# Kernel optimization log

Measured on AMD Instinct MI355X. Metric: run time of the kernel, lower is better.

Reference implementation:

```python
import jax, jax.numpy as jnp
import numpy as np

N = 9            # digits
NC = N * N       # 81 cells
H = 128          # hidden1
B = 2048         # batch of puzzles


def _constraint_mask():
    idx = np.arange(NC)
    r, c = idx // N, idx % N
    cm = np.zeros((3, NC, NC), np.float32)
    cm[0] = (r[:, None] == r[None, :])
    cm[1] = (c[:, None] == c[None, :])
    cm[2] = ((r[:, None] // 3 == r[None, :] // 3) & (c[:, None] // 3 == c[None, :] // 3))
    return cm


def setup_inputs() -> dict:
    key = jax.random.key(0)
    k1, k2, k3, k4 = jax.random.split(key, 4)
    digits = jax.random.randint(k1, (B, NC), 0, N)
    given = (jax.random.uniform(k2, (B, NC)) < 0.45).astype(jnp.float32)
    x = jax.nn.one_hot(digits, N, dtype=jnp.float32) * given[:, :, None]
    W1 = jax.random.normal(k3, (H, 3 * N), jnp.float32) * 0.05  # torch Linear weight [out,in]
    W2 = jax.random.normal(k4, (N, H), jnp.float32) * 0.05
    return {"x": x, "W1": W1, "W2": W2,
            "constraint_mask": jnp.asarray(_constraint_mask())}


def reference(x, W1, W2, constraint_mask):
    bts = x.shape[0]
    bidx = jnp.arange(bts)

    def step(carry, _):
        xc, x_pred = carry
        # constraints[b,r,q,e] = sum_k cm[r,q,k] * x[b,k,e]   (same math as
        # (x.unsqueeze(1).unsqueeze(1) * c).sum(dim=3), without the 5D temp)
        cons = jnp.einsum('rqk,bke->brqe', constraint_mask, xc)
        f = cons.reshape(bts, NC, 3 * N)          # matches torch row-major reshape
        empty = (xc.sum(-1) == 0)                 # [b,81] empty-cell mask
        h = jax.nn.relu(f @ W1.T)                 # [b,81,H]
        y = h @ W2.T                              # [b,81,9]
        s_full = jax.nn.softmax(y, axis=-1)       # softmax over digit dim
        x_pred = jnp.where(empty[:, :, None], s_full, x_pred)
        s = jnp.where(empty[:, :, None], s_full, 0.0)
        score = s.max(-1)                         # [b,81]
        pos = s.argmax(-1)                        # [b,81] best digit per cell
        mmax = score.argmax(-1)                   # [b] most confident cell
        has_empty = empty.any(-1)                 # [b] boards with work left
        digit = pos[bidx, mmax]                   # [b]
        upd = (jax.nn.one_hot(mmax, NC, dtype=xc.dtype)[:, :, None]
               * jax.nn.one_hot(digit, N, dtype=xc.dtype)[:, None, :])
        upd = upd * has_empty[:, None, None].astype(xc.dtype)
        xc = jnp.where(upd > 0, jnp.asarray(1.0, xc.dtype), xc)  # index_put_ of ones
        return (xc, x_pred), None

    # original loops min_empty (<=81) times; iterations past min_empty are no-ops
    (xf, x_pred), _ = jax.lax.scan(step, (x, x), None, length=NC)
    return x_pred
```

## Files before the change

### kernel.cpp

```cpp
#include <hip/hip_runtime.h>
#include <cstdint>


__device__ __forceinline__ void wave_fence() {
  asm volatile("s_waitcnt lgkmcnt(0)" ::: "memory");
}

template <int CTRL>
__device__ __forceinline__ float dppf(float v) {
  return __int_as_float(__builtin_amdgcn_update_dpp(
      0, __float_as_int(v), CTRL, 0xF, 0xF, true));
}
template <int IMM>
__device__ __forceinline__ float swzf(float v) {
  return __int_as_float(__builtin_amdgcn_ds_swizzle(__float_as_int(v), IMM));
}
__device__ __forceinline__ float redmax16(float v) {
  v = fmaxf(v, dppf<0xB1>(v));
  v = fmaxf(v, dppf<0x4E>(v));
  v = fmaxf(v, swzf<0x101F>(v));
  v = fmaxf(v, dppf<0x128>(v));
  return v;
}
__device__ __forceinline__ float redsum16(float v) {
  v += dppf<0xB1>(v);
  v += dppf<0x4E>(v);
  v += swzf<0x101F>(v);
  v += dppf<0x128>(v);
  return v;
}
__device__ __forceinline__ float redmax64(float v) {
  v = fmaxf(v, dppf<0xB1>(v));
  v = fmaxf(v, dppf<0x4E>(v));
  v = fmaxf(v, swzf<0x101F>(v));
  v = fmaxf(v, dppf<0x128>(v));
  v = fmaxf(v, swzf<0x401F>(v));
  v = fmaxf(v, __shfl_xor(v, 32));
  return v;
}

__device__ __forceinline__ int dist_row(int i) {
  int r = i / 27;
  int t = i - 27 * r;
  if (r == 0) return t / 3;
  if (r == 1) return 9 + (t % 3);
  return 12 + 3 * (t / 9) + (t % 3);
}

__global__ __launch_bounds__(64, 2)
void sudoku_solver(const float* __restrict__ x, const float* __restrict__ W1g,
                   const float* __restrict__ W2g, float* __restrict__ out) {
  __shared__ float W2s[9][132];
  __shared__ float cnt[3][9][12];
  __shared__ float hbuf[3][132];
  __shared__ float sful[21][12];
  __shared__ float rscore[21];
  __shared__ int   rargs[21];
  __shared__ int   digc[81];

  const int lane = threadIdx.x;
  const int b = blockIdx.x;
  const float* xb = x + b * 729;
  float* ob = out + b * 729;

  for (int idx = lane; idx < 1152; idx += 64)
    W2s[idx >> 7][idx & 127] = W2g[idx];

  float w1a[27], w1b[27];
  #pragma unroll
  for (int c = 0; c < 27; ++c) {
    w1a[c] = W1g[lane * 27 + c];
    w1b[c] = W1g[(lane + 64) * 27 + c];
  }

  for (int idx = lane; idx < 3 * 9 * 12; idx += 64)
    ((float*)cnt)[idx] = 0.f;

  bool eA, eB = false;
  {
    float v[9]; int dg = -1;
    #pragma unroll
    for (int e = 0; e < 9; ++e) v[e] = xb[lane * 9 + e];
    #pragma unroll
    for (int e = 0; e < 9; ++e) { if (v[e] > 0.5f) dg = e; ob[lane * 9 + e] = v[e]; }
    eA = (dg < 0); digc[lane] = dg;
    if (lane < 17) {
      const int i2 = 64 + lane;
      float w[9]; int dg2 = -1;
      #pragma unroll
      for (int e = 0; e < 9; ++e) w[e] = xb[i2 * 9 + e];
      #pragma unroll
      for (int e = 0; e < 9; ++e) { if (w[e] > 0.5f) dg2 = e; ob[i2 * 9 + e] = w[e]; }
      eB = (dg2 < 0); digc[i2] = dg2;
    }
  }
  const int distA = dist_row(lane);
  const int distB = (lane < 17) ? dist_row(64 + lane) : 0;
  wave_fence();

  if (lane < 27) {
    const int g = lane / 9, gi = lane - 9 * g;
    float c9[9];
    #pragma unroll
    for (int e = 0; e < 9; ++e) c9[e] = 0.f;
    #pragma unroll
    for (int k = 0; k < 9; ++k) {
      int cell;
      if (g == 0)      cell = gi * 9 + k;
      else if (g == 1) cell = k * 9 + gi;
      else             cell = (gi / 3) * 27 + (gi % 3) * 3 + (k / 3) * 9 + (k % 3);
      const int dg = digc[cell];
      #pragma unroll
      for (int e = 0; e < 9; ++e) c9[e] += (dg == e) ? 1.f : 0.f;
    }
    #pragma unroll
    for (int e = 0; e < 9; ++e) cnt[g][gi][e] = c9[e];
  }
  wave_fence();

  const int rr3 = lane >> 4;
  const int dl  = lane & 15;
  const bool dval = (rr3 < 3) && (dl < 9);
  const float* hrow = hbuf[(rr3 < 3) ? rr3 : 0];
  const float* wrow = W2s[(dl < 9) ? dl : 0];

  auto update_rows = [&](int u0, int u1, int u2) {
    #pragma unroll
    for (int rr = 0; rr < 3; ++rr) {
      const int u = (rr == 0) ? u0 : (rr == 1) ? u1 : u2;
      int g, gia, gib, gic;
      if (u < 9)       { g = 0; gia = gib = gic = u; }
      else if (u < 12) { g = 1; gia = 3 * (u - 9); gib = gia + 1; gic = gia + 2; }
      else             { g = 2; gia = gib = gic = u - 12; }
      const float* f0 = &cnt[g][gia][0];
      const float* f1 = &cnt[g][gib][0];
      const float* f2 = &cnt[g][gic][0];
      float acc0 = 0.f, acc1 = 0.f;
#define DOT9(FP, BASE)                                                          \
      {                                                                         \
        float4 fA = *(const float4*)(FP);                                       \
        float4 fB = *(const float4*)((FP) + 4);                                 \
        float f8 = (FP)[8];                                                     \
        acc0 = fmaf(fA.x, w1a[BASE+0], acc0); acc1 = fmaf(fA.x, w1b[BASE+0], acc1); \
        acc0 = fmaf(fA.y, w1a[BASE+1], acc0); acc1 = fmaf(fA.y, w1b[BASE+1], acc1); \
        acc0 = fmaf(fA.z, w1a[BASE+2], acc0); acc1 = fmaf(fA.z, w1b[BASE+2], acc1); \
        acc0 = fmaf(fA.w, w1a[BASE+3], acc0); acc1 = fmaf(fA.w, w1b[BASE+3], acc1); \
        acc0 = fmaf(fB.x, w1a[BASE+4], acc0); acc1 = fmaf(fB.x, w1b[BASE+4], acc1); \
        acc0 = fmaf(fB.y, w1a[BASE+5], acc0); acc1 = fmaf(fB.y, w1b[BASE+5], acc1); \
        acc0 = fmaf(fB.z, w1a[BASE+6], acc0); acc1 = fmaf(fB.z, w1b[BASE+6], acc1); \
        acc0 = fmaf(fB.w, w1a[BASE+7], acc0); acc1 = fmaf(fB.w, w1b[BASE+7], acc1); \
        acc0 = fmaf(f8,  w1a[BASE+8], acc0);  acc1 = fmaf(f8,  w1b[BASE+8], acc1);  \
      }
      DOT9(f0, 0)
      DOT9(f1, 9)
      DOT9(f2, 18)
#undef DOT9
      hbuf[rr][lane]      = fmaxf(acc0, 0.f);
      hbuf[rr][64 + lane] = fmaxf(acc1, 0.f);
    }
    wave_fence();

    float a0 = 0.f, a1 = 0.f, a2 = 0.f, a3 = 0.f;
    const float4* hp = (const float4*)hrow;
    const float4* wp = (const float4*)wrow;
    #pragma unroll
    for (int k = 0; k < 32; k += 4) {
      float4 h0 = hp[k],     ww0 = wp[k];
      float4 h1 = hp[k + 1], ww1 = wp[k + 1];
      float4 h2 = hp[k + 2], ww2 = wp[k + 2];
      float4 h3 = hp[k + 3], ww3 = wp[k + 3];
      a0 = fmaf(h0.x, ww0.x, a0); a0 = fmaf(h0.y, ww0.y, a0);
      a0 = fmaf(h0.z, ww0.z, a0); a0 = fmaf(h0.w, ww0.w, a0);
      a1 = fmaf(h1.x, ww1.x, a1); a1 = fmaf(h1.y, ww1.y, a1);
      a1 = fmaf(h1.z, ww1.z, a1); a1 = fmaf(h1.w, ww1.w, a1);
      a2 = fmaf(h2.x, ww2.x, a2); a2 = fmaf(h2.y, ww2.y, a2);
      a2 = fmaf(h2.z, ww2.z, a2); a2 = fmaf(h2.w, ww2.w, a2);
      a3 = fmaf(h3.x, ww3.x, a3); a3 = fmaf(h3.y, ww3.y, a3);
      a3 = fmaf(h3.z, ww3.z, a3); a3 = fmaf(h3.w, ww3.w, a3);
    }
    float y = (a0 + a1) + (a2 + a3);
    y = dval ? y : -1e30f;
    const float ymax = redmax16(y);
    const float ev = dval ? expf(y - ymax) : 0.f;
    const float S = redsum16(ev);
    const float s = ev / S;
    const float sm = dval ? s : 0.f;
    const float rmax = redmax16(sm);
    unsigned long long bm = __ballot(dval && (sm == rmax));
    const int u = (rr3 == 0) ? u0 : (rr3 == 1) ? u1 : u2;
    if (dval) sful[u][dl] = s;
    if (rr3 < 3 && dl == 0) {
      rscore[u] = rmax;
      rargs[u] = __builtin_ctz((unsigned)((bm >> (rr3 * 16)) & 0xFFFFull));
    }
    wave_fence();
  };

  #pragma unroll 1
  for (int p = 0; p < 7; ++p) update_rows(3 * p, 3 * p + 1, 3 * p + 2);

  #pragma unroll 1
  for (int step = 0; step < 81; ++step) {
    const float sA = eA ? rscore[distA] : 0.f;
    const float sB = (lane < 17 && eB) ? rscore[distB] : 0.f;
    const float M = redmax64(fmaxf(sA, sB));
    if (M <= 0.f) break;

    const unsigned long long m0 = __ballot(sA == M);
    const unsigned long long m1 = __ballot((lane < 17) && (sB == M));
    const int mmax = m0 ? __builtin_ctzll(m0) : 64 + __builtin_ctzll(m1);

    const int du = dist_row(mmax);
    const int r = mmax / 9, c = mmax - 9 * r;
    const int bx = (mmax / 27) * 3 + c / 3;
    const int digit = rargs[du];

    if (lane < 3) {
      const int gi = (lane == 0) ? r : (lane == 1) ? c : bx;
      cnt[lane][gi][digit] += 1.f;
    } else if (lane >= 8 && lane < 17) {
      ob[mmax * 9 + (lane - 8)] = sful[du][lane - 8];
    }
    if (lane == mmax) eA = false;
    if (lane + 64 == mmax) eB = false;
    wave_fence();

    update_rows(r, 9 + c / 3, 12 + bx);
  }
}

extern "C" void kernel_launch(void* const* d_in, const int* in_sizes, int n_in,
                              void* d_out, int out_size, void* d_ws, size_t ws_size,
                              hipStream_t stream) {
  const float* x  = (const float*)d_in[0];
  const float* W1 = (const float*)d_in[1];
  const float* W2 = (const float*)d_in[2];
  float* out = (float*)d_out;
  sudoku_solver<<<dim3(2048), dim3(64), 0, stream>>>(x, W1, W2, out);
}
```

Baseline: 242.3 us.

## Incrementally update hidden pre-activations and register-resident W2 reductions with fp64 tie resolution

Caches layer-1 pre-activations per distinct row class in shared memory and updates them by adding the W1 column of the placed digit, instead of recomputing the 27-wide dot product each step. W2 is held in registers, and the second layer becomes cross-lane reductions, so scores and argmax digits stay in registers rather than shared memory. Near-ties within a threshold are re-resolved with an fp64 recompute so the chosen cell and digit match the reference. This adds complexity, a heavier rarely-taken double-precision path, and a risk that incremental float accumulation drifts from a full recompute.

```diff
diff --git a/kernel.cpp b/kernel.cpp
--- a/kernel.cpp
+++ b/kernel.cpp
@@ -1,10 +1,12 @@
 #include <hip/hip_runtime.h>
 #include <cstdint>
+#include <cmath>
 
 
 __device__ __forceinline__ void wave_fence() {
   asm volatile("s_waitcnt lgkmcnt(0)" ::: "memory");
 }
+__device__ __forceinline__ void cbar() { asm volatile("" ::: "memory"); }
 
 template <int CTRL>
 __device__ __forceinline__ float dppf(float v) {
@@ -14,20 +16,6 @@
 template <int IMM>
 __device__ __forceinline__ float swzf(float v) {
   return __int_as_float(__builtin_amdgcn_ds_swizzle(__float_as_int(v), IMM));
-}
-__device__ __forceinline__ float redmax16(float v) {
-  v = fmaxf(v, dppf<0xB1>(v));
-  v = fmaxf(v, dppf<0x4E>(v));
-  v = fmaxf(v, swzf<0x101F>(v));
-  v = fmaxf(v, dppf<0x128>(v));
-  return v;
-}
-__device__ __forceinline__ float redsum16(float v) {
-  v += dppf<0xB1>(v);
-  v += dppf<0x4E>(v);
-  v += swzf<0x101F>(v);
-  v += dppf<0x128>(v);
-  return v;
 }
 __device__ __forceinline__ float redmax64(float v) {
   v = fmaxf(v, dppf<0xB1>(v));
@@ -47,16 +35,23 @@
   return 12 + 3 * (t / 9) + (t % 3);
 }
 
+#define SEL9C(A, B)                                                          \
+  (b3d ? A[(B) + 8]                                                          \
+       : (b2d ? (b1d ? (b0d ? A[(B) + 7] : A[(B) + 6])                       \
+                     : (b0d ? A[(B) + 5] : A[(B) + 4]))                      \
+              : (b1d ? (b0d ? A[(B) + 3] : A[(B) + 2])                       \
+                     : (b0d ? A[(B) + 1] : A[(B) + 0]))))
+
 __global__ __launch_bounds__(64, 2)
 void sudoku_solver(const float* __restrict__ x, const float* __restrict__ W1g,
                    const float* __restrict__ W2g, float* __restrict__ out) {
-  __shared__ float W2s[9][132];
-  __shared__ float cnt[3][9][12];
-  __shared__ float hbuf[3][132];
-  __shared__ float sful[21][12];
-  __shared__ float rscore[21];
-  __shared__ int   rargs[21];
-  __shared__ int   digc[81];
+  __shared__ float  preL[21][128];
+  __shared__ float  W2s[9][132];
+  __shared__ float  sful[21][12];
+  __shared__ float  cnt[3][9][12];
+  __shared__ float  rgapL[24];
+  __shared__ double h64[128];
+  __shared__ int    digc[81];
 
   const int lane = threadIdx.x;
   const int b = blockIdx.x;
@@ -72,6 +67,12 @@
     w1a[c] = W1g[lane * 27 + c];
     w1b[c] = W1g[(lane + 64) * 27 + c];
   }
+  float w2A[9], w2B[9];
+  #pragma unroll
+  for (int d = 0; d < 9; ++d) {
+    w2A[d] = W2g[d * 128 + lane];
+    w2B[d] = W2g[d * 128 + 64 + lane];
+  }
 
   for (int idx = lane; idx < 3 * 9 * 12; idx += 64)
     ((float*)cnt)[idx] = 0.f;
@@ -95,7 +96,12 @@
     }
   }
   const int distA = dist_row(lane);
-  const int distB = (lane < 17) ? dist_row(64 + lane) : 0;
+  const int distB = (lane < 17) ? dist_row(64 + lane) : 255;
+  const int rr3 = lane >> 4;
+  const int dl  = lane & 15;
+  const bool sv = (rr3 < 3) && (dl < 9);
+  const bool sb0 = dl & 1, sb1 = dl & 2, sb2 = dl & 4, sb3 = dl & 8;
+  const int bpaddr = ((lane ^ 32) & 63) << 2;
   wave_fence();
 
   if (lane < 27) {
@@ -118,102 +124,244 @@
   }
   wave_fence();
 
-  const int rr3 = lane >> 4;
-  const int dl  = lane & 15;
-  const bool dval = (rr3 < 3) && (dl < 9);
-  const float* hrow = hbuf[(rr3 < 3) ? rr3 : 0];
-  const float* wrow = W2s[(dl < 9) ? dl : 0];
-
-  auto update_rows = [&](int u0, int u1, int u2) {
+  float myscoreA = 0.f, myscoreB = 0.f;
+  int mydigA = 0, mydigB = 0;
+  float hA[3], hB[3];
+
+  auto grp_map = [](int u, int& g, int& gia, int& gib, int& gic) {
+    if (u < 9)       { g = 0; gia = gib = gic = u; }
+    else if (u < 12) { g = 1; gia = 3 * (u - 9); gib = gia + 1; gic = gia + 2; }
+    else             { g = 2; gia = gib = gic = u - 12; }
+  };
+
+  auto phaseD = [&](int u0, int u1, int u2) {
+    float P[3][9];
+    #pragma unroll
+    for (int rr = 0; rr < 3; ++rr)
+      #pragma unroll
+      for (int dd = 0; dd < 9; ++dd)
+        P[rr][dd] = fmaf(hA[rr], w2A[dd], hB[rr] * w2B[dd]);
+    #pragma unroll
+    for (int rr = 0; rr < 3; ++rr)
+      #pragma unroll
+      for (int dd = 0; dd < 9; ++dd) {
+        float v = P[rr][dd];
+        v += swzf<0x401F>(v);
+        v += __int_as_float(__builtin_amdgcn_ds_bpermute(bpaddr, __float_as_int(v)));
+        v = v + dppf<0x121>(v);
+        v = v + dppf<0x122>(v);
+        v = v + dppf<0x124>(v);
+        v = v + dppf<0x128>(v);
+        P[rr][dd] = v;
+      }
+    float q[9];
+    #pragma unroll
+    for (int dd = 0; dd < 9; ++dd)
+      q[dd] = (rr3 >= 2) ? P[2][dd] : ((rr3 == 1) ? P[1][dd] : P[0][dd]);
+    float ymax = q[0];
+    #pragma unroll
+    for (int dd = 1; dd < 9; ++dd) ymax = fmaxf(ymax, q[dd]);
+    float e[9];
+    #pragma unroll
+    for (int dd = 0; dd < 9; ++dd) e[dd] = __expf(q[dd] - ymax);
+    float S = e[0];
+    #pragma unroll
+    for (int dd = 1; dd < 9; ++dd) S += e[dd];
+    const float rinv = 1.0f / S;
+    float s[9];
+    #pragma unroll
+    for (int dd = 0; dd < 9; ++dd) s[dd] = e[dd] * rinv;
+    float smax = s[0], s2nd = -1.f; int sarg = 0;
+    #pragma unroll
+    for (int dd = 1; dd < 9; ++dd) {
+      const bool g = s[dd] > smax;
+      s2nd = g ? smax : ((s[dd] > s2nd) ? s[dd] : s2nd);
+      smax = g ? s[dd] : smax;
+      sarg = g ? dd : sarg;
+    }
+    {
+      float x01 = sb0 ? s[1] : s[0], x23 = sb0 ? s[3] : s[2];
+      float x45 = sb0 ? s[5] : s[4], x67 = sb0 ? s[7] : s[6];
+      float y03 = sb1 ? x23 : x01, y47 = sb1 ? x67 : x45;
+      float z07 = sb2 ? y47 : y03;
+      float ssel = sb3 ? s[8] : z07;
+      int usel = (rr3 == 1) ? u1 : ((rr3 == 2) ? u2 : u0);
+      if (sv) sful[usel][dl] = ssel;
+      if (rr3 < 3 && dl == 0) rgapL[usel] = smax - s2nd;
+    }
+    const float sc0 = __int_as_float(__builtin_amdgcn_readlane(__float_as_int(smax), 0));
+    const float sc1 = __int_as_float(__builtin_amdgcn_readlane(__float_as_int(smax), 16));
+    const float sc2 = __int_as_float(__builtin_amdgcn_readlane(__float_as_int(smax), 32));
+    const int a0 = __builtin_amdgcn_readlane(sarg, 0);
+    const int a1 = __builtin_amdgcn_readlane(sarg, 16);
+    const int a2 = __builtin_amdgcn_readlane(sarg, 32);
+    myscoreA = (distA == u0) ? sc0 : myscoreA;
+    myscoreA = (distA == u1) ? sc1 : myscoreA;
+    myscoreA = (distA == u2) ? sc2 : myscoreA;
+    mydigA   = (distA == u0) ? a0 : mydigA;
+    mydigA   = (distA == u1) ? a1 : mydigA;
+    mydigA   = (distA == u2) ? a2 : mydigA;
+    myscoreB = (distB == u0) ? sc0 : myscoreB;
+    myscoreB = (distB == u1) ? sc1 : myscoreB;
+    myscoreB = (distB == u2) ? sc2 : myscoreB;
+    mydigB   = (distB == u0) ? a0 : mydigB;
+    mydigB   = (distB == u1) ? a1 : mydigB;
+    mydigB   = (distB == u2) ? a2 : mydigB;
+    cbar();
+  };
+
+  auto resolve_row = [&](int u, int& dig) -> double {
+    int g, gia, gib, gic;
+    grp_map(u, g, gia, gib, gic);
+    const float* f0 = &cnt[g][gia][0];
+    const float* f1 = &cnt[g][gib][0];
+    const float* f2 = &cnt[g][gic][0];
+    double p0 = 0.0, p1 = 0.0;
+    #pragma unroll
+    for (int c = 0; c < 9; ++c) {
+      const double fv = (double)f0[c];
+      p0 = fma(fv, (double)w1a[c], p0); p1 = fma(fv, (double)w1b[c], p1);
+    }
+    #pragma unroll
+    for (int c = 0; c < 9; ++c) {
+      const double fv = (double)f1[c];
+      p0 = fma(fv, (double)w1a[9 + c], p0); p1 = fma(fv, (double)w1b[9 + c], p1);
+    }
+    #pragma unroll
+    for (int c = 0; c < 9; ++c) {
+      const double fv = (double)f2[c];
+      p0 = fma(fv, (double)w1a[18 + c], p0); p1 = fma(fv, (double)w1b[18 + c], p1);
+    }
+    h64[lane]      = fmax(p0, 0.0);
+    h64[64 + lane] = fmax(p1, 0.0);
+    wave_fence();
+    double y = -1e300;
+    if (lane < 9) {
+      double acc = 0.0;
+      const double2* hp = (const double2*)h64;
+      const float4* wp = (const float4*)&W2s[lane][0];
+      #pragma unroll 4
+      for (int k = 0; k < 32; ++k) {
+        const double2 a = hp[2 * k];
+        const double2 c2 = hp[2 * k + 1];
+        const float4 w = wp[k];
+        acc = fma(a.x,  (double)w.x, acc);
+        acc = fma(a.y,  (double)w.y, acc);
+        acc = fma(c2.x, (double)w.z, acc);
+        acc = fma(c2.y, (double)w.w, acc);
+      }
+      y = acc;
+    }
+    double ymax = y;
+    #pragma unroll
+    for (int m = 1; m < 64; m <<= 1) ymax = fmax(ymax, __shfl_xor(ymax, m));
+    const double ev = (lane < 9) ? exp(y - ymax) : 0.0;
+    double S = ev;
+    #pragma unroll
+    for (int m = 1; m < 64; m <<= 1) S += __shfl_xor(S, m);
+    const double s = (lane < 9) ? (ev / S) : -1.0;
+    double smax = s;
+    #pragma unroll
+    for (int m = 1; m < 64; m <<= 1) smax = fmax(smax, __shfl_xor(smax, m));
+    const unsigned long long bm = __ballot(s == smax);
+    dig = __builtin_ctzll(bm);
+    return smax;
+  };
+
+  #pragma unroll 1
+  for (int p = 0; p < 7; ++p) {
+    const int U0 = 3 * p;
     #pragma unroll
     for (int rr = 0; rr < 3; ++rr) {
-      const int u = (rr == 0) ? u0 : (rr == 1) ? u1 : u2;
+      const int u = U0 + rr;
       int g, gia, gib, gic;
-      if (u < 9)       { g = 0; gia = gib = gic = u; }
-      else if (u < 12) { g = 1; gia = 3 * (u - 9); gib = gia + 1; gic = gia + 2; }
-      else             { g = 2; gia = gib = gic = u - 12; }
+      grp_map(u, g, gia, gib, gic);
       const float* f0 = &cnt[g][gia][0];
       const float* f1 = &cnt[g][gib][0];
       const float* f2 = &cnt[g][gic][0];
       float acc0 = 0.f, acc1 = 0.f;
-#define DOT9(FP, BASE)                                                          \
-      {                                                                         \
-        float4 fA = *(const float4*)(FP);                                       \
-        float4 fB = *(const float4*)((FP) + 4);                                 \
-        float f8 = (FP)[8];                                                     \
-        acc0 = fmaf(fA.x, w1a[BASE+0], acc0); acc1 = fmaf(fA.x, w1b[BASE+0], acc1); \
-        acc0 = fmaf(fA.y, w1a[BASE+1], acc0); acc1 = fmaf(fA.y, w1b[BASE+1], acc1); \
-        acc0 = fmaf(fA.z, w1a[BASE+2], acc0); acc1 = fmaf(fA.z, w1b[BASE+2], acc1); \
-        acc0 = fmaf(fA.w, w1a[BASE+3], acc0); acc1 = fmaf(fA.w, w1b[BASE+3], acc1); \
-        acc0 = fmaf(fB.x, w1a[BASE+4], acc0); acc1 = fmaf(fB.x, w1b[BASE+4], acc1); \
-        acc0 = fmaf(fB.y, w1a[BASE+5], acc0); acc1 = fmaf(fB.y, w1b[BASE+5], acc1); \
-        acc0 = fmaf(fB.z, w1a[BASE+6], acc0); acc1 = fmaf(fB.z, w1b[BASE+6], acc1); \
-        acc0 = fmaf(fB.w, w1a[BASE+7], acc0); acc1 = fmaf(fB.w, w1b[BASE+7], acc1); \
-        acc0 = fmaf(f8,  w1a[BASE+8], acc0);  acc1 = fmaf(f8,  w1b[BASE+8], acc1);  \
-      }
-      DOT9(f0, 0)
-      DOT9(f1, 9)
-      DOT9(f2, 18)
-#undef DOT9
-      hbuf[rr][lane]      = fmaxf(acc0, 0.f);
-      hbuf[rr][64 + lane] = fmaxf(acc1, 0.f);
-    }
-    wave_fence();
-
-    float a0 = 0.f, a1 = 0.f, a2 = 0.f, a3 = 0.f;
-    const float4* hp = (const float4*)hrow;
-    const float4* wp = (const float4*)wrow;
-    #pragma unroll
-    for (int k = 0; k < 32; k += 4) {
-      float4 h0 = hp[k],     ww0 = wp[k];
-      float4 h1 = hp[k + 1], ww1 = wp[k + 1];
-      float4 h2 = hp[k + 2], ww2 = wp[k + 2];
-      float4 h3 = hp[k + 3], ww3 = wp[k + 3];
-      a0 = fmaf(h0.x, ww0.x, a0); a0 = fmaf(h0.y, ww0.y, a0);
-      a0 = fmaf(h0.z, ww0.z, a0); a0 = fmaf(h0.w, ww0.w, a0);
-      a1 = fmaf(h1.x, ww1.x, a1); a1 = fmaf(h1.y, ww1.y, a1);
-      a1 = fmaf(h1.z, ww1.z, a1); a1 = fmaf(h1.w, ww1.w, a1);
-      a2 = fmaf(h2.x, ww2.x, a2); a2 = fmaf(h2.y, ww2.y, a2);
-      a2 = fmaf(h2.z, ww2.z, a2); a2 = fmaf(h2.w, ww2.w, a2);
-      a3 = fmaf(h3.x, ww3.x, a3); a3 = fmaf(h3.y, ww3.y, a3);
-      a3 = fmaf(h3.z, ww3.z, a3); a3 = fmaf(h3.w, ww3.w, a3);
-    }
-    float y = (a0 + a1) + (a2 + a3);
-    y = dval ? y : -1e30f;
-    const float ymax = redmax16(y);
-    const float ev = dval ? expf(y - ymax) : 0.f;
-    const float S = redsum16(ev);
-    const float s = ev / S;
-    const float sm = dval ? s : 0.f;
-    const float rmax = redmax16(sm);
-    unsigned long long bm = __ballot(dval && (sm == rmax));
-    const int u = (rr3 == 0) ? u0 : (rr3 == 1) ? u1 : u2;
-    if (dval) sful[u][dl] = s;
-    if (rr3 < 3 && dl == 0) {
-      rscore[u] = rmax;
-      rargs[u] = __builtin_ctz((unsigned)((bm >> (rr3 * 16)) & 0xFFFFull));
-    }
-    wave_fence();
-  };
-
-  #pragma unroll 1
-  for (int p = 0; p < 7; ++p) update_rows(3 * p, 3 * p + 1, 3 * p + 2);
+      #pragma unroll
+      for (int c = 0; c < 9; ++c) {
+        acc0 = fmaf(f0[c], w1a[c], acc0); acc1 = fmaf(f0[c], w1b[c], acc1);
+      }
+      #pragma unroll
+      for (int c = 0; c < 9; ++c) {
+        acc0 = fmaf(f1[c], w1a[9 + c], acc0); acc1 = fmaf(f1[c], w1b[9 + c], acc1);
+      }
+      #pragma unroll
+      for (int c = 0; c < 9; ++c) {
+        acc0 = fmaf(f2[c], w1a[18 + c], acc0); acc1 = fmaf(f2[c], w1b[18 + c], acc1);
+      }
+      float2 pw; pw.x = acc0; pw.y = acc1;
+      *(float2*)&preL[u][2 * lane] = pw;
+      hA[rr] = fmaxf(acc0, 0.f);
+      hB[rr] = fmaxf(acc1, 0.f);
+    }
+    cbar();
+    phaseD(U0, U0 + 1, U0 + 2);
+  }
+
+  const float THR = 1e-3f;
 
   #pragma unroll 1
   for (int step = 0; step < 81; ++step) {
-    const float sA = eA ? rscore[distA] : 0.f;
-    const float sB = (lane < 17 && eB) ? rscore[distB] : 0.f;
+    const float sA = eA ? myscoreA : 0.f;
+    const float sB = (lane < 17 && eB) ? myscoreB : 0.f;
     const float M = redmax64(fmaxf(sA, sB));
     if (M <= 0.f) break;
 
-    const unsigned long long m0 = __ballot(sA == M);
-    const unsigned long long m1 = __ballot((lane < 17) && (sB == M));
-    const int mmax = m0 ? __builtin_ctzll(m0) : 64 + __builtin_ctzll(m1);
+    const bool cA = (sA > 0.f) && (sA >= M - THR);
+    const bool cB = (sB > 0.f) && (sB >= M - THR);
+    const unsigned long long candA = __ballot(cA);
+    const unsigned long long candB = __ballot(cB) & 0x1FFFFull;
+    const int firstC = candA ? __builtin_ctzll(candA) : 64 + __builtin_ctzll(candB);
+    const int uf = dist_row(firstC);
+    const unsigned long long diffA = __ballot(cA && (distA != uf));
+    const unsigned long long diffB = __ballot(cB && (distB != uf));
+    const bool multirow = (diffA | diffB) != 0ull;
+
+    int mmax, digit;
+    if (!multirow) {
+      mmax = firstC;
+      const float gap = rgapL[uf];
+      if (gap > THR) {
+        const int dA_ = __builtin_amdgcn_readlane(mydigA, mmax & 63);
+        const int dB_ = __builtin_amdgcn_readlane(mydigB, mmax & 63);
+        digit = (mmax < 64) ? dA_ : dB_;
+      } else {
+        resolve_row(uf, digit);
+      }
+    } else {
+      double csA = -1.0, csB = -1.0;
+      int dgA = 0, dgB = 0;
+      unsigned long long mA = candA, mB = candB;
+      #pragma unroll 1
+      while (mA | mB) {
+        const int idx = mA ? __builtin_ctzll(mA) : 64 + __builtin_ctzll(mB);
+        const int u = dist_row(idx);
+        int dg;
+        const double sc = resolve_row(u, dg);
+        const bool hitA = ((mA >> lane) & 1ull) && (distA == u);
+        const bool hitB = (lane < 17) && ((mB >> lane) & 1ull) && (distB == u);
+        if (hitA) { csA = sc; dgA = dg; }
+        if (hitB) { csB = sc; dgB = dg; }
+        mA &= ~__ballot(hitA);
+        mB &= ~(__ballot(hitB) & 0x1FFFFull);
+      }
+      double mm = fmax(csA, csB);
+      #pragma unroll
+      for (int m = 1; m < 64; m <<= 1) mm = fmax(mm, __shfl_xor(mm, m));
+      const unsigned long long wAm = __ballot(csA == mm);
+      const unsigned long long wBm = __ballot((lane < 17) && (csB == mm));
+      mmax = wAm ? __builtin_ctzll(wAm) : 64 + __builtin_ctzll(wBm);
+      digit = (mmax < 64) ? __builtin_amdgcn_readlane(dgA, mmax)
+                          : __builtin_amdgcn_readlane(dgB, mmax - 64);
+    }
 
     const int du = dist_row(mmax);
     const int r = mmax / 9, c = mmax - 9 * r;
     const int bx = (mmax / 27) * 3 + c / 3;
-    const int digit = rargs[du];
+    const int q3 = c - 3 * (c / 3);
 
     if (lane < 3) {
       const int gi = (lane == 0) ? r : (lane == 1) ? c : bx;
@@ -225,7 +373,29 @@
     if (lane + 64 == mmax) eB = false;
     wave_fence();
 
-    update_rows(r, 9 + c / 3, 12 + bx);
+    const int u0 = r, u1 = 9 + c / 3, u2 = 12 + bx;
+    {
+      const bool b0d = digit & 1, b1d = digit & 2, b2d = digit & 4, b3d = digit & 8;
+      const float ca0 = SEL9C(w1a, 0), ca1 = SEL9C(w1a, 9), ca2 = SEL9C(w1a, 18);
+      const float cb0 = SEL9C(w1b, 0), cb1 = SEL9C(w1b, 9), cb2 = SEL9C(w1b, 18);
+      const float d02a = ca0 + ca1 + ca2, d02b = cb0 + cb1 + cb2;
+      const float d1a = (q3 == 0) ? ca0 : ((q3 == 1) ? ca1 : ca2);
+      const float d1b = (q3 == 0) ? cb0 : ((q3 == 1) ? cb1 : cb2);
+      float2 p0 = *(float2*)&preL[u0][2 * lane];
+      float2 p1 = *(float2*)&preL[u1][2 * lane];
+      float2 p2 = *(float2*)&preL[u2][2 * lane];
+      p0.x += d02a; p0.y += d02b;
+      p1.x += d1a;  p1.y += d1b;
+      p2.x += d02a; p2.y += d02b;
+      *(float2*)&preL[u0][2 * lane] = p0;
+      *(float2*)&preL[u1][2 * lane] = p1;
+      *(float2*)&preL[u2][2 * lane] = p2;
+      hA[0] = fmaxf(p0.x, 0.f); hB[0] = fmaxf(p0.y, 0.f);
+      hA[1] = fmaxf(p1.x, 0.f); hB[1] = fmaxf(p1.y, 0.f);
+      hA[2] = fmaxf(p2.x, 0.f); hB[2] = fmaxf(p2.y, 0.f);
+    }
+    cbar();
+    phaseD(u0, u1, u2);
   }
 }
 
```

New measurement: 481.8 us. +98.8%, slower.

## Switch solver MLP and softmax to double precision with register-held W2

Applied to the files above, without the earlier changes.

Recomputes the hidden layer, output projection and softmax in fp64. W2 now sits in per-lane double registers and each lane writes partial products to a shared fp64 buffer, which are then summed per output slot. Row scores are held in registers and reduced with shuffles instead of the DPP/swizzle paths and shared score arrays. The intent is mainly to make argmax tie-breaking match the reference. The cost is much slower fp64 arithmetic, a 64-term serial LDS reduction per slot, and more LDS traffic and register pressure.

```diff
diff --git a/kernel.cpp b/kernel.cpp
--- a/kernel.cpp
+++ b/kernel.cpp
@@ -1,42 +1,10 @@
 #include <hip/hip_runtime.h>
 #include <cstdint>
+#include <cmath>
 
 
 __device__ __forceinline__ void wave_fence() {
   asm volatile("s_waitcnt lgkmcnt(0)" ::: "memory");
-}
-
-template <int CTRL>
-__device__ __forceinline__ float dppf(float v) {
-  return __int_as_float(__builtin_amdgcn_update_dpp(
-      0, __float_as_int(v), CTRL, 0xF, 0xF, true));
-}
-template <int IMM>
-__device__ __forceinline__ float swzf(float v) {
-  return __int_as_float(__builtin_amdgcn_ds_swizzle(__float_as_int(v), IMM));
-}
-__device__ __forceinline__ float redmax16(float v) {
-  v = fmaxf(v, dppf<0xB1>(v));
-  v = fmaxf(v, dppf<0x4E>(v));
-  v = fmaxf(v, swzf<0x101F>(v));
-  v = fmaxf(v, dppf<0x128>(v));
-  return v;
-}
-__device__ __forceinline__ float redsum16(float v) {
-  v += dppf<0xB1>(v);
-  v += dppf<0x4E>(v);
-  v += swzf<0x101F>(v);
-  v += dppf<0x128>(v);
-  return v;
-}
-__device__ __forceinline__ float redmax64(float v) {
-  v = fmaxf(v, dppf<0xB1>(v));
-  v = fmaxf(v, dppf<0x4E>(v));
-  v = fmaxf(v, swzf<0x101F>(v));
-  v = fmaxf(v, dppf<0x128>(v));
-  v = fmaxf(v, swzf<0x401F>(v));
-  v = fmaxf(v, __shfl_xor(v, 32));
-  return v;
 }
 
 __device__ __forceinline__ int dist_row(int i) {
@@ -50,21 +18,16 @@
 __global__ __launch_bounds__(64, 2)
 void sudoku_solver(const float* __restrict__ x, const float* __restrict__ W1g,
                    const float* __restrict__ W2g, float* __restrict__ out) {
-  __shared__ float W2s[9][132];
-  __shared__ float cnt[3][9][12];
-  __shared__ float hbuf[3][132];
-  __shared__ float sful[21][12];
-  __shared__ float rscore[21];
-  __shared__ int   rargs[21];
-  __shared__ int   digc[81];
+  __shared__ double pp[27][65];
+  __shared__ float  cnt[3][9][12];
+  __shared__ float  sful[21][12];
+  __shared__ int    rargsL[24];
+  __shared__ int    digc[81];
 
   const int lane = threadIdx.x;
   const int b = blockIdx.x;
   const float* xb = x + b * 729;
   float* ob = out + b * 729;
-
-  for (int idx = lane; idx < 1152; idx += 64)
-    W2s[idx >> 7][idx & 127] = W2g[idx];
 
   float w1a[27], w1b[27];
   #pragma unroll
@@ -72,6 +35,12 @@
     w1a[c] = W1g[lane * 27 + c];
     w1b[c] = W1g[(lane + 64) * 27 + c];
   }
+  double w2Ad[9], w2Bd[9];
+  #pragma unroll
+  for (int d = 0; d < 9; ++d) {
+    w2Ad[d] = (double)W2g[d * 128 + lane];
+    w2Bd[d] = (double)W2g[d * 128 + 64 + lane];
+  }
 
   for (int idx = lane; idx < 3 * 9 * 12; idx += 64)
     ((float*)cnt)[idx] = 0.f;
@@ -95,7 +64,11 @@
     }
   }
   const int distA = dist_row(lane);
-  const int distB = (lane < 17) ? dist_row(64 + lane) : 0;
+  const int distB = (lane < 17) ? dist_row(64 + lane) : 255;
+  const int rr3 = lane >> 4;
+  const int dl  = lane & 15;
+  const bool sv = (rr3 < 3) && (dl < 9);
+  const int slot = rr3 * 9 + dl;
   wave_fence();
 
   if (lane < 27) {
@@ -118,13 +91,10 @@
   }
   wave_fence();
 
-  const int rr3 = lane >> 4;
-  const int dl  = lane & 15;
-  const bool dval = (rr3 < 3) && (dl < 9);
-  const float* hrow = hbuf[(rr3 < 3) ? rr3 : 0];
-  const float* wrow = W2s[(dl < 9) ? dl : 0];
+  double myscoreA = 0.0, myscoreB = 0.0;
 
   auto update_rows = [&](int u0, int u1, int u2) {
+    double hA[3], hB[3];
     #pragma unroll
     for (int rr = 0; rr < 3; ++rr) {
       const int u = (rr == 0) ? u0 : (rr == 1) ? u1 : u2;
@@ -135,64 +105,72 @@
       const float* f0 = &cnt[g][gia][0];
       const float* f1 = &cnt[g][gib][0];
       const float* f2 = &cnt[g][gic][0];
-      float acc0 = 0.f, acc1 = 0.f;
-#define DOT9(FP, BASE)                                                          \
-      {                                                                         \
-        float4 fA = *(const float4*)(FP);                                       \
-        float4 fB = *(const float4*)((FP) + 4);                                 \
-        float f8 = (FP)[8];                                                     \
-        acc0 = fmaf(fA.x, w1a[BASE+0], acc0); acc1 = fmaf(fA.x, w1b[BASE+0], acc1); \
-        acc0 = fmaf(fA.y, w1a[BASE+1], acc0); acc1 = fmaf(fA.y, w1b[BASE+1], acc1); \
-        acc0 = fmaf(fA.z, w1a[BASE+2], acc0); acc1 = fmaf(fA.z, w1b[BASE+2], acc1); \
-        acc0 = fmaf(fA.w, w1a[BASE+3], acc0); acc1 = fmaf(fA.w, w1b[BASE+3], acc1); \
-        acc0 = fmaf(fB.x, w1a[BASE+4], acc0); acc1 = fmaf(fB.x, w1b[BASE+4], acc1); \
-        acc0 = fmaf(fB.y, w1a[BASE+5], acc0); acc1 = fmaf(fB.y, w1b[BASE+5], acc1); \
-        acc0 = fmaf(fB.z, w1a[BASE+6], acc0); acc1 = fmaf(fB.z, w1b[BASE+6], acc1); \
-        acc0 = fmaf(fB.w, w1a[BASE+7], acc0); acc1 = fmaf(fB.w, w1b[BASE+7], acc1); \
-        acc0 = fmaf(f8,  w1a[BASE+8], acc0);  acc1 = fmaf(f8,  w1b[BASE+8], acc1);  \
+      double a0 = 0.0, a1 = 0.0;
+      #pragma unroll
+      for (int c = 0; c < 9; ++c) {
+        const double fv = (double)f0[c];
+        a0 = fma(fv, (double)w1a[c], a0); a1 = fma(fv, (double)w1b[c], a1);
       }
-      DOT9(f0, 0)
-      DOT9(f1, 9)
-      DOT9(f2, 18)
-#undef DOT9
-      hbuf[rr][lane]      = fmaxf(acc0, 0.f);
-      hbuf[rr][64 + lane] = fmaxf(acc1, 0.f);
-    }
+      #pragma unroll
+      for (int c = 0; c < 9; ++c) {
+        const double fv = (double)f1[c];
+        a0 = fma(fv, (double)w1a[9 + c], a0); a1 = fma(fv, (double)w1b[9 + c], a1);
+      }
+      #pragma unroll
+      for (int c = 0; c < 9; ++c) {
+        const double fv = (double)f2[c];
+        a0 = fma(fv, (double)w1a[18 + c], a0); a1 = fma(fv, (double)w1b[18 + c], a1);
+      }
+      hA[rr] = fmax(a0, 0.0);
+      hB[rr] = fmax(a1, 0.0);
+    }
+
+    #pragma unroll
+    for (int rr = 0; rr < 3; ++rr)
+      #pragma unroll
+      for (int dd = 0; dd < 9; ++dd)
+        pp[rr * 9 + dd][lane] = fma(hA[rr], w2Ad[dd], hB[rr] * w2Bd[dd]);
     wave_fence();
 
-    float a0 = 0.f, a1 = 0.f, a2 = 0.f, a3 = 0.f;
-    const float4* hp = (const float4*)hrow;
-    const float4* wp = (const float4*)wrow;
-    #pragma unroll
-    for (int k = 0; k < 32; k += 4) {
-      float4 h0 = hp[k],     ww0 = wp[k];
-      float4 h1 = hp[k + 1], ww1 = wp[k + 1];
-      float4 h2 = hp[k + 2], ww2 = wp[k + 2];
-      float4 h3 = hp[k + 3], ww3 = wp[k + 3];
-      a0 = fmaf(h0.x, ww0.x, a0); a0 = fmaf(h0.y, ww0.y, a0);
-      a0 = fmaf(h0.z, ww0.z, a0); a0 = fmaf(h0.w, ww0.w, a0);
-      a1 = fmaf(h1.x, ww1.x, a1); a1 = fmaf(h1.y, ww1.y, a1);
-      a1 = fmaf(h1.z, ww1.z, a1); a1 = fmaf(h1.w, ww1.w, a1);
-      a2 = fmaf(h2.x, ww2.x, a2); a2 = fmaf(h2.y, ww2.y, a2);
-      a2 = fmaf(h2.z, ww2.z, a2); a2 = fmaf(h2.w, ww2.w, a2);
-      a3 = fmaf(h3.x, ww3.x, a3); a3 = fmaf(h3.y, ww3.y, a3);
-      a3 = fmaf(h3.z, ww3.z, a3); a3 = fmaf(h3.w, ww3.w, a3);
-    }
-    float y = (a0 + a1) + (a2 + a3);
-    y = dval ? y : -1e30f;
-    const float ymax = redmax16(y);
-    const float ev = dval ? expf(y - ymax) : 0.f;
-    const float S = redsum16(ev);
-    const float s = ev / S;
-    const float sm = dval ? s : 0.f;
-    const float rmax = redmax16(sm);
-    unsigned long long bm = __ballot(dval && (sm == rmax));
-    const int u = (rr3 == 0) ? u0 : (rr3 == 1) ? u1 : u2;
-    if (dval) sful[u][dl] = s;
-    if (rr3 < 3 && dl == 0) {
-      rscore[u] = rmax;
-      rargs[u] = __builtin_ctz((unsigned)((bm >> (rr3 * 16)) & 0xFFFFull));
-    }
+    double y = -1.0e300;
+    if (sv) {
+      double acc = 0.0;
+      #pragma unroll 16
+      for (int g = 0; g < 64; ++g) acc += pp[slot][g];
+      y = acc;
+    }
+
+    double ymax = y;
+    ymax = fmax(ymax, __shfl_xor(ymax, 1));
+    ymax = fmax(ymax, __shfl_xor(ymax, 2));
+    ymax = fmax(ymax, __shfl_xor(ymax, 4));
+    ymax = fmax(ymax, __shfl_xor(ymax, 8));
+    const double ev = sv ? exp(y - ymax) : 0.0;
+    double S = ev;
+    S += __shfl_xor(S, 1);
+    S += __shfl_xor(S, 2);
+    S += __shfl_xor(S, 4);
+    S += __shfl_xor(S, 8);
+    const double s = ev / S;
+    const double scmp = sv ? s : -1.0;
+    double smax = scmp;
+    smax = fmax(smax, __shfl_xor(smax, 1));
+    smax = fmax(smax, __shfl_xor(smax, 2));
+    smax = fmax(smax, __shfl_xor(smax, 4));
+    smax = fmax(smax, __shfl_xor(smax, 8));
+    const unsigned long long bm = __ballot(scmp == smax);
+    const int u_sel = (rr3 == 1) ? u1 : ((rr3 == 2) ? u2 : u0);
+    if (sv) sful[u_sel][dl] = (float)s;
+    if (rr3 < 3 && dl == 0)
+      rargsL[u_sel] = __builtin_ctz((unsigned)((bm >> (rr3 * 16)) & 0x1FFu));
+
+    const double sc0 = __shfl(smax, 0);
+    const double sc1 = __shfl(smax, 16);
+    const double sc2 = __shfl(smax, 32);
+    myscoreA = (distA == u0) ? sc0 : (distA == u1) ? sc1
+             : (distA == u2) ? sc2 : myscoreA;
+    myscoreB = (distB == u0) ? sc0 : (distB == u1) ? sc1
+             : (distB == u2) ? sc2 : myscoreB;
     wave_fence();
   };
 
@@ -201,19 +179,25 @@
 
   #pragma unroll 1
   for (int step = 0; step < 81; ++step) {
-    const float sA = eA ? rscore[distA] : 0.f;
-    const float sB = (lane < 17 && eB) ? rscore[distB] : 0.f;
-    const float M = redmax64(fmaxf(sA, sB));
-    if (M <= 0.f) break;
+    const double sA = eA ? myscoreA : 0.0;
+    const double sB = (lane < 17 && eB) ? myscoreB : 0.0;
+    double M = fmax(sA, sB);
+    M = fmax(M, __shfl_xor(M, 1));
+    M = fmax(M, __shfl_xor(M, 2));
+    M = fmax(M, __shfl_xor(M, 4));
+    M = fmax(M, __shfl_xor(M, 8));
+    M = fmax(M, __shfl_xor(M, 16));
+    M = fmax(M, __shfl_xor(M, 32));
+    if (M <= 0.0) break;
 
     const unsigned long long m0 = __ballot(sA == M);
     const unsigned long long m1 = __ballot((lane < 17) && (sB == M));
     const int mmax = m0 ? __builtin_ctzll(m0) : 64 + __builtin_ctzll(m1);
 
     const int du = dist_row(mmax);
+    const int digit = rargsL[du];
     const int r = mmax / 9, c = mmax - 9 * r;
     const int bx = (mmax / 27) * 3 + c / 3;
-    const int digit = rargs[du];
 
     if (lane < 3) {
       const int gi = (lane == 0) ? r : (lane == 1) ? c : bx;
```

Measured after the change: 301.1 us. 24.3% more time.
